# Performance work log

Measured on AMD Instinct MI355X. Metric: run time of the kernel, lower is better.

Reference implementation:

```python
import jax, jax.numpy as jnp
import numpy as np
import math

B = 2048
NOSC = 64            # oscillators per modality
M = 3                # modalities (audio, text, vision) in sorted order
BDIM = 256           # binding_dim
DT = 0.01
NSTEPS = 10
DIMS = [512, 768, 1024]  # audio, text, vision
TWO_PI = 2.0 * math.pi


def setup_inputs() -> dict:
    key = jax.random.key(0)
    ks = iter(jax.random.split(key, 40))
    d = {}
    names = ['a', 't', 'v']
    for name, dim, x_key in zip(names, DIMS, ['x_audio', 'x_text', 'x_vision']):
        d[x_key] = jax.random.normal(next(ks), (B, dim), dtype=jnp.float32)
        s = 1.0 / math.sqrt(dim)
        d[f'Wf_{name}'] = jax.random.uniform(next(ks), (BDIM, dim), jnp.float32, -s, s)
        d[f'bf_{name}'] = jax.random.uniform(next(ks), (BDIM,), jnp.float32, -s, s)
        d[f'Wp_{name}'] = jax.random.uniform(next(ks), (NOSC, dim), jnp.float32, -s, s)
        d[f'bp_{name}'] = jax.random.uniform(next(ks), (NOSC,), jnp.float32, -s, s)
    # omegas: randn*0.1 + 1.0 + i*0.5 for i-th sorted modality
    for i, name in enumerate(names):
        d[f'omega_{name}'] = jax.random.normal(next(ks), (NOSC,), jnp.float32) * 0.1 + 1.0 + i * 0.5
    N = M * NOSC
    d['inter_coupling'] = jax.random.normal(next(ks), (N, N), jnp.float32) * 0.1
    s = 1.0 / math.sqrt(BDIM * M)
    d['W_fusion'] = jax.random.uniform(next(ks), (BDIM, BDIM * M), jnp.float32, -s, s)
    d['b_fusion'] = jax.random.uniform(next(ks), (BDIM,), jnp.float32, -s, s)
    return d


def reference(x_audio, x_text, x_vision,
              Wf_a, bf_a, Wp_a, bp_a,
              Wf_t, bf_t, Wp_t, bp_t,
              Wf_v, bf_v, Wp_v, bp_v,
              omega_a, omega_t, omega_v,
              inter_coupling, W_fusion, b_fusion):
    def enc(x, Wf, bf, Wp, bp):
        encoded = x @ Wf.T + bf                       # (B, BDIM)
        phases = (x @ Wp.T + bp) % TWO_PI             # (B, NOSC)
        return encoded, phases

    e_a, p_a = enc(x_audio, Wf_a, bf_a, Wp_a, bp_a)
    e_t, p_t = enc(x_text, Wf_t, bf_t, Wp_t, bp_t)
    e_v, p_v = enc(x_vision, Wf_v, bf_v, Wp_v, bp_v)

    phases = jnp.concatenate([p_a, p_t, p_v], axis=-1)        # (B, N)
    omega = jnp.concatenate([omega_a, omega_t, omega_v])      # (N,)
    K = (inter_coupling + inter_coupling.T) * 0.5             # (N, N)
    N = phases.shape[-1]

    def step(ph, _):
        diff = ph[:, :, None] - ph[:, None, :]                # (B, N, N)
        forces = jnp.einsum('ij,bij->bi', K, jnp.sin(diff)) / N
        ph = (ph + DT * (omega[None, :] + forces)) % TWO_PI
        return ph, None

    phases, _ = jax.lax.scan(step, phases, None, length=NSTEPS)

    pm = [phases[:, i * NOSC:(i + 1) * NOSC] for i in range(M)]  # per-modality

    # PLV between banks a,b: |mean_{i,j} exp(i(a_i - b_j))| = R_a * R_b where
    # R = |mean_k exp(i phi_k)| (resultant length), computed with real math.
    R = jnp.stack([jnp.sqrt(jnp.mean(jnp.cos(p), -1) ** 2 +
                            jnp.mean(jnp.sin(p), -1) ** 2) for p in pm])  # (M, B)
    bm = jnp.mean(R[:, None, :] * R[None, :, :], axis=-1)      # (M, M)
    binding_matrix = jnp.where(jnp.eye(M, dtype=bool), 1.0, bm)

    fused_parts = []
    for e, p in zip([e_a, e_t, e_v], pm):
        phase_mod = jnp.mean(jnp.cos(p), axis=-1, keepdims=True)  # (B, 1)
        fused_parts.append(e * (0.5 + 0.5 * phase_mod))
    fused = jnp.concatenate(fused_parts, axis=-1)              # (B, M*BDIM)
    bound = fused @ W_fusion.T + b_fusion                      # (B, BDIM)

    triu = jnp.triu(jnp.ones((M, M), dtype=bool), k=1)
    total = jnp.sum(jnp.where(triu, binding_matrix, 0.0)) / triu.sum()
    total_binding = jnp.full((bound.shape[0],), total)

    return bound, binding_matrix, phases, total_binding
```

## Files before the change

kernel.cpp:

```cpp
#include <hip/hip_runtime.h>
#include <math.h>

typedef short bf16x8 __attribute__((ext_vector_type(8)));
typedef short bf16x4 __attribute__((ext_vector_type(4)));
typedef float f32x4  __attribute__((ext_vector_type(4)));

#define INV_2PI  0.15915494309189535f
#define TWO_PI_F 6.283185307179586f
#define FSCALE   8.2893199e-06f

static __device__ inline short f2bf(float f) {
    union { float f; unsigned u; } v; v.f = f;
    unsigned r = (v.u + 0x7FFFu + ((v.u >> 16) & 1u)) >> 16;
    return (short)r;
}
static __device__ inline float bf2f(short h) {
    union { unsigned u; float f; } v; v.u = ((unsigned)(unsigned short)h) << 16;
    return v.f;
}

__global__ __launch_bounds__(256) void front_kernel(
    const float* __restrict__ xa, const float* __restrict__ xt, const float* __restrict__ xv,
    const float* __restrict__ Wpa, const float* __restrict__ Wpt, const float* __restrict__ Wpv,
    const float* __restrict__ Wfa, const float* __restrict__ Wft, const float* __restrict__ Wfv,
    const float* __restrict__ Wfu,
    const float* __restrict__ IC,
    const float* __restrict__ oa, const float* __restrict__ ot, const float* __restrict__ ov,
    const float* __restrict__ bpa, const float* __restrict__ bpt, const float* __restrict__ bpv,
    float* __restrict__ partial, short* __restrict__ XB, short* __restrict__ WB,
    short* __restrict__ Kp,
    float* __restrict__ om_eff, float* __restrict__ bp_all, float* __restrict__ bacc)
{
    __shared__ alignas(16) float As[16][72];
    __shared__ alignas(16) float Bs[16][72];
    int b = blockIdx.x;
    int t = threadIdx.x;

    if (b < 576) {
        int slot = b % 18, rb = b / 18;
        int z = slot < 4 ? 0 : (slot < 10 ? 1 : 2);
        int chunk = slot - (z == 0 ? 0 : (z == 1 ? 4 : 10));
        const float* A = z == 0 ? xa : (z == 1 ? xt : xv);
        const float* W = z == 0 ? Wpa : (z == 1 ? Wpt : Wpv);
        short* XBz = XB + (z == 0 ? 0 : (z == 1 ? 1048576 : 2621440));
        int K = z == 0 ? 512 : (z == 1 ? 768 : 1024);
        int kb = chunk * 128;
        int m0 = rb * 64;

        int tx = t & 15, ty = t >> 4;
        int row = t >> 2, c4 = t & 3;

        float acc[4][4] = {};
        float4 ar = *(const float4*)&A[(size_t)(m0 + row) * K + kb + c4 * 4];
        float4 br = *(const float4*)&W[(size_t)row * K + kb + c4 * 4];

        for (int k0 = 0; k0 < 128; k0 += 16) {
            if (k0) __syncthreads();
            As[c4 * 4 + 0][row] = ar.x;
            As[c4 * 4 + 1][row] = ar.y;
            As[c4 * 4 + 2][row] = ar.z;
            As[c4 * 4 + 3][row] = ar.w;
            Bs[c4 * 4 + 0][row] = br.x;
            Bs[c4 * 4 + 1][row] = br.y;
            Bs[c4 * 4 + 2][row] = br.z;
            Bs[c4 * 4 + 3][row] = br.w;
            {
                bf16x4 h; h[0] = f2bf(ar.x); h[1] = f2bf(ar.y);
                h[2] = f2bf(ar.z); h[3] = f2bf(ar.w);
                *(bf16x4*)&XBz[(size_t)(m0 + row) * K + kb + k0 + c4 * 4] = h;
            }
            __syncthreads();
            if (k0 + 16 < 128) {
                ar = *(const float4*)&A[(size_t)(m0 + row) * K + kb + k0 + 16 + c4 * 4];
                br = *(const float4*)&W[(size_t)row * K + kb + k0 + 16 + c4 * 4];
            }
#pragma unroll
            for (int kk = 0; kk < 16; ++kk) {
                float4 aq = *(const float4*)&As[kk][ty * 4];
                float4 bq = *(const float4*)&Bs[kk][tx * 4];
                float av[4] = {aq.x, aq.y, aq.z, aq.w};
                float bv[4] = {bq.x, bq.y, bq.z, bq.w};
#pragma unroll
                for (int i = 0; i < 4; ++i)
#pragma unroll
                    for (int j = 0; j < 4; ++j)
                        acc[i][j] += av[i] * bv[j];
            }
        }

        float* P = partial + (size_t)slot * 131072;
#pragma unroll
        for (int i = 0; i < 4; ++i) {
            float4 v = make_float4(acc[i][0], acc[i][1], acc[i][2], acc[i][3]);
            *(float4*)&P[(size_t)(m0 + ty * 4 + i) * 64 + tx * 4] = v;
        }
    } else if (b < 600) {
        for (int u = (b - 576) * 256 + t; u < 196608; u += 24 * 256) {
            const float4* sp;
            if (u < 32768)       sp = (const float4*)Wfa + u;
            else if (u < 81920)  sp = (const float4*)Wft + (u - 32768);
            else if (u < 147456) sp = (const float4*)Wfv + (u - 81920);
            else                 sp = (const float4*)Wfu + (u - 147456);
            float4 v = *sp;
            bf16x4 h; h[0] = f2bf(v.x); h[1] = f2bf(v.y); h[2] = f2bf(v.z); h[3] = f2bf(v.w);
            *(bf16x4*)(WB + (size_t)u * 4) = h;
        }
    } else if (b < 632) {
        for (int idx = (b - 600) * 256 + t; idx < 36864; idx += 32 * 256) {
            int k = idx / 192, n = idx - k * 192;
            float v = 0.5f * (IC[k * 192 + n] + IC[n * 192 + k]);
            int nt = n >> 4, kc = k >> 5;
            int lane = ((k >> 3) & 3) * 16 + (n & 15);
            int j = k & 7;
            Kp[((nt * 6 + kc) * 64 + lane) * 8 + j] = f2bf(v);
        }
    } else {
        if (t < 192) {
            float w = t < 64 ? oa[t] : (t < 128 ? ot[t - 64] : ov[t - 128]);
            om_eff[t] = w * (0.01f * INV_2PI);
            float bb = t < 64 ? bpa[t] : (t < 128 ? bpt[t - 64] : bpv[t - 128]);
            bp_all[t] = bb;
        }
        if (t < 4) bacc[t] = 0.f;
    }
}

__global__ __launch_bounds__(256) void mid_kernel(
    const short* __restrict__ XB, const short* __restrict__ WB,
    const float* __restrict__ ba, const float* __restrict__ bt, const float* __restrict__ bv,
    const float* __restrict__ partial, const float* __restrict__ bp_all,
    const short* __restrict__ Kp, const float* __restrict__ om_eff,
    short* __restrict__ e_bf16,
    float* __restrict__ phases_out, float* __restrict__ pm, float* __restrict__ bacc)
{
    __shared__ alignas(16) char smem[27840];
    int b = blockIdx.x;
    int t = threadIdx.x;
    int lane = t & 63, w = t >> 6;
    int q = lane >> 4, col = lane & 15;

    if (b < 384) {
        int z = b / 128, r = b % 128;
        int m0 = (r >> 2) * 64, n0 = (r & 3) * 64;
        const short* A    = XB + (z == 0 ? 0 : (z == 1 ? 1048576 : 2621440));
        const short* W    = WB + (z == 0 ? 0 : (z == 1 ? 131072 : 327680));
        const float* bias = z == 0 ? ba : (z == 1 ? bt : bv);
        int K             = z == 0 ? 512 : (z == 1 ? 768 : 1024);

        short* As = (short*)smem;
        short* Bs = (short*)smem + 64 * 72;

        int srow = t >> 3, sc8 = t & 7;

        f32x4 acc[4];
#pragma unroll
        for (int f = 0; f < 4; ++f)
#pragma unroll
            for (int rr = 0; rr < 4; ++rr) acc[f][rr] = 0.f;

        bf16x8 av[2], bv8[2];
#pragma unroll
        for (int p = 0; p < 2; ++p) {
            av[p]  = *(const bf16x8*)&A[(size_t)(m0 + srow + 32 * p) * K + sc8 * 8];
            bv8[p] = *(const bf16x8*)&W[(size_t)(n0 + srow + 32 * p) * K + sc8 * 8];
        }

        for (int kb = 0; kb < K; kb += 64) {
            if (kb) __syncthreads();
#pragma unroll
            for (int p = 0; p < 2; ++p) {
                *(bf16x8*)&As[(srow + 32 * p) * 72 + sc8 * 8] = av[p];
                *(bf16x8*)&Bs[(srow + 32 * p) * 72 + sc8 * 8] = bv8[p];
            }
            __syncthreads();
            if (kb + 64 < K) {
#pragma unroll
                for (int p = 0; p < 2; ++p) {
                    av[p]  = *(const bf16x8*)&A[(size_t)(m0 + srow + 32 * p) * K + kb + 64 + sc8 * 8];
                    bv8[p] = *(const bf16x8*)&W[(size_t)(n0 + srow + 32 * p) * K + kb + 64 + sc8 * 8];
                }
            }

            bf16x8 bfr[2];
#pragma unroll
            for (int kc = 0; kc < 2; ++kc)
                bfr[kc] = *(const bf16x8*)&Bs[(w * 16 + col) * 72 + kc * 32 + q * 8];
#pragma unroll
            for (int f = 0; f < 4; ++f)
#pragma unroll
                for (int kc = 0; kc < 2; ++kc) {
                    bf16x8 af = *(const bf16x8*)&As[(f * 16 + col) * 72 + kc * 32 + q * 8];
                    acc[f] = __builtin_amdgcn_mfma_f32_16x16x32_bf16(af, bfr[kc], acc[f], 0, 0, 0);
                }
        }

        int n = n0 + w * 16 + col;
        float bn = bias[n];
#pragma unroll
        for (int f = 0; f < 4; ++f)
#pragma unroll
            for (int rr = 0; rr < 4; ++rr) {
                int m = m0 + f * 16 + q * 4 + rr;
                e_bf16[(size_t)m * 768 + z * 256 + n] = f2bf(acc[f][rr] + bn);
            }
    } else {
        short (*cs)[2][16][216] = (short (*)[2][16][216])smem;
        float (*Rl)[3] = (float (*)[3])(smem + 27648);

        int m0 = (b - 384) * 16;

        bf16x8 kb[3][6];
#pragma unroll
        for (int ntl = 0; ntl < 3; ++ntl)
#pragma unroll
            for (int kc = 0; kc < 6; ++kc) {
                int nt = w * 3 + ntl;
                kb[ntl][kc] = *(const bf16x8*)&Kp[((nt * 6 + kc) * 64 + lane) * 8];
            }

        float ph[3][4], om[3], c[3][4], s[3][4];
#pragma unroll
        for (int ntl = 0; ntl < 3; ++ntl) {
            int i = (w * 3 + ntl) * 16 + col;
            int z = i >> 6;
            int c0 = (z == 0) ? 0 : (z == 1 ? 4 : 10);
            int nch = (z == 0) ? 4 : (z == 1 ? 6 : 8);
            om[ntl] = om_eff[i];
#pragma unroll
            for (int r = 0; r < 4; ++r) {
                float raw = bp_all[i];
                size_t base = (size_t)c0 * 131072 + (size_t)(m0 + q * 4 + r) * 64 + (i & 63);
#pragma unroll
                for (int cc = 0; cc < 8; ++cc)
                    if (cc < nch) raw += partial[base + (size_t)cc * 131072];
                raw *= INV_2PI;
                ph[ntl][r] = raw - floorf(raw);
            }
        }

        for (int step = 0; step < 10; ++step) {
            int p = step & 1;
#pragma unroll
            for (int ntl = 0; ntl < 3; ++ntl) {
                int i = (w * 3 + ntl) * 16 + col;
#pragma unroll
                for (int r = 0; r < 4; ++r) {
                    c[ntl][r] = __builtin_amdgcn_cosf(ph[ntl][r]);
                    s[ntl][r] = __builtin_amdgcn_sinf(ph[ntl][r]);
                    cs[p][0][q * 4 + r][i] = f2bf(c[ntl][r]);
                    cs[p][1][q * 4 + r][i] = f2bf(s[ntl][r]);
                }
            }
            __syncthreads();

            f32x4 aC[3], aS[3];
#pragma unroll
            for (int ntl = 0; ntl < 3; ++ntl)
#pragma unroll
                for (int r = 0; r < 4; ++r) { aC[ntl][r] = 0.f; aS[ntl][r] = 0.f; }

#pragma unroll
            for (int kc = 0; kc < 6; ++kc) {
                bf16x8 ac  = *(const bf16x8*)&cs[p][0][col][kc * 32 + q * 8];
                bf16x8 as_ = *(const bf16x8*)&cs[p][1][col][kc * 32 + q * 8];
#pragma unroll
                for (int ntl = 0; ntl < 3; ++ntl) {
                    aC[ntl] = __builtin_amdgcn_mfma_f32_16x16x32_bf16(ac,  kb[ntl][kc], aC[ntl], 0, 0, 0);
                    aS[ntl] = __builtin_amdgcn_mfma_f32_16x16x32_bf16(as_, kb[ntl][kc], aS[ntl], 0, 0, 0);
                }
            }

#pragma unroll
            for (int ntl = 0; ntl < 3; ++ntl)
#pragma unroll
                for (int r = 0; r < 4; ++r) {
                    float f = (s[ntl][r] * aC[ntl][r] - c[ntl][r] * aS[ntl][r]) * FSCALE;
                    float pn = ph[ntl][r] + om[ntl] + f;
                    ph[ntl][r] = pn - floorf(pn);
                }
        }

#pragma unroll
        for (int ntl = 0; ntl < 3; ++ntl) {
            int i = (w * 3 + ntl) * 16 + col;
#pragma unroll
            for (int r = 0; r < 4; ++r) {
                float cp = __builtin_amdgcn_cosf(ph[ntl][r]);
                float sp = __builtin_amdgcn_sinf(ph[ntl][r]);
                cs[0][0][q * 4 + r][i] = f2bf(cp);
                cs[0][1][q * 4 + r][i] = f2bf(sp);
                phases_out[(size_t)(m0 + q * 4 + r) * 192 + i] = ph[ntl][r] * TWO_PI_F;
            }
        }
        __syncthreads();

        if (t < 48) {
            int r = t & 15, mod = t >> 4;
            float sc = 0.f, ss = 0.f;
#pragma unroll
            for (int g = 0; g < 8; ++g) {
                bf16x8 vc = *(const bf16x8*)&cs[0][0][r][mod * 64 + g * 8];
                bf16x8 vs = *(const bf16x8*)&cs[0][1][r][mod * 64 + g * 8];
#pragma unroll
                for (int j = 0; j < 8; ++j) { sc += bf2f(vc[j]); ss += bf2f(vs[j]); }
            }
            sc *= (1.f / 64.f); ss *= (1.f / 64.f);
            pm[(size_t)(m0 + r) * 3 + mod] = 0.5f + 0.5f * sc;
            Rl[r][mod] = sqrtf(sc * sc + ss * ss);
        }
        __syncthreads();
        if (t < 3) {
            int a = (t == 2) ? 1 : 0;
            int bb = (t == 0) ? 1 : 2;
            float accp = 0.f;
            for (int r = 0; r < 16; ++r) accp += Rl[r][a] * Rl[r][bb];
            atomicAdd(&bacc[t], accp);
        }
    }
}

__global__ __launch_bounds__(256) void back_kernel(
    const short* __restrict__ e_bf16, const short* __restrict__ WB,
    const float* __restrict__ bias, const float* __restrict__ pm,
    const float* __restrict__ bacc,
    float* __restrict__ out_bound, float* __restrict__ out_bm, float* __restrict__ out_total)
{
    const short* Wfb = WB + 589824;
    __shared__ alignas(16) short As2[16 * 776];

    int m0 = blockIdx.x * 16, n0 = blockIdx.y * 128;
    int t = threadIdx.x;
    int lane = t & 63, w = t >> 6;
    int q = lane >> 4, col = lane & 15;

#pragma unroll
    for (int i = 0; i < 6; ++i) {
        int g = t + 256 * i;
        int rw = g / 96, cg = g - rw * 96;
        float sc = pm[(size_t)(m0 + rw) * 3 + (cg >> 5)];
        bf16x8 v = *(const bf16x8*)&e_bf16[(size_t)(m0 + rw) * 768 + cg * 8];
        bf16x8 h;
#pragma unroll
        for (int j = 0; j < 8; ++j) h[j] = f2bf(bf2f(v[j]) * sc);
        *(bf16x8*)&As2[rw * 776 + cg * 8] = h;
    }
    __syncthreads();

    f32x4 facc[2];
#pragma unroll
    for (int j = 0; j < 2; ++j)
#pragma unroll
        for (int rr = 0; rr < 4; ++rr) facc[j][rr] = 0.f;

    int n_[2];
#pragma unroll
    for (int j = 0; j < 2; ++j) n_[j] = n0 + (w * 2 + j) * 16 + col;

    bf16x8 bcur[2], bnxt[2];
#pragma unroll
    for (int j = 0; j < 2; ++j)
        bcur[j] = *(const bf16x8*)&Wfb[(size_t)n_[j] * 768 + q * 8];

    for (int k0 = 0; k0 < 768; k0 += 32) {
        if (k0 + 32 < 768) {
#pragma unroll
            for (int j = 0; j < 2; ++j)
                bnxt[j] = *(const bf16x8*)&Wfb[(size_t)n_[j] * 768 + k0 + 32 + q * 8];
        }
        bf16x8 af = *(const bf16x8*)&As2[col * 776 + k0 + q * 8];
#pragma unroll
        for (int j = 0; j < 2; ++j)
            facc[j] = __builtin_amdgcn_mfma_f32_16x16x32_bf16(af, bcur[j], facc[j], 0, 0, 0);
#pragma unroll
        for (int j = 0; j < 2; ++j) bcur[j] = bnxt[j];
    }

#pragma unroll
    for (int j = 0; j < 2; ++j) {
        float bn = bias[n_[j]];
#pragma unroll
        for (int rr = 0; rr < 4; ++rr) {
            int m = m0 + q * 4 + rr;
            out_bound[(size_t)m * 256 + n_[j]] = facc[j][rr] + bn;
        }
    }

    if (blockIdx.x == 0 && blockIdx.y == 0) {
        float p01 = bacc[0] * (1.f / 2048.f);
        float p02 = bacc[1] * (1.f / 2048.f);
        float p12 = bacc[2] * (1.f / 2048.f);
        float total = (p01 + p02 + p12) * (1.f / 3.f);
        if (t == 0) {
            out_bm[0] = 1.f; out_bm[1] = p01; out_bm[2] = p02;
            out_bm[3] = p01; out_bm[4] = 1.f; out_bm[5] = p12;
            out_bm[6] = p02; out_bm[7] = p12; out_bm[8] = 1.f;
        }
        for (int i = t; i < 2048; i += 256) out_total[i] = total;
    }
}

extern "C" void kernel_launch(void* const* d_in, const int* in_sizes, int n_in,
                              void* d_out, int out_size, void* d_ws, size_t ws_size,
                              hipStream_t stream)
{
    const float* x_a  = (const float*)d_in[0];
    const float* Wf_a = (const float*)d_in[1];
    const float* bf_a = (const float*)d_in[2];
    const float* Wp_a = (const float*)d_in[3];
    const float* bp_a = (const float*)d_in[4];
    const float* x_t  = (const float*)d_in[5];
    const float* Wf_t = (const float*)d_in[6];
    const float* bf_t = (const float*)d_in[7];
    const float* Wp_t = (const float*)d_in[8];
    const float* bp_t = (const float*)d_in[9];
    const float* x_v  = (const float*)d_in[10];
    const float* Wf_v = (const float*)d_in[11];
    const float* bf_v = (const float*)d_in[12];
    const float* Wp_v = (const float*)d_in[13];
    const float* bp_v = (const float*)d_in[14];
    const float* om_a = (const float*)d_in[15];
    const float* om_t = (const float*)d_in[16];
    const float* om_v = (const float*)d_in[17];
    const float* IC   = (const float*)d_in[18];
    const float* Wfu  = (const float*)d_in[19];
    const float* bfu  = (const float*)d_in[20];

    float* ws      = (float*)d_ws;
    float* omw     = ws;
    float* bpw     = ws + 256;
    float* pmv     = ws + 512;
    float* baccw   = ws + 6656;
    float* partial = ws + 6720;
    short* e_bf    = (short*)(ws + 2366016);
    short* XB      = (short*)(ws + 3152448);
    short* Kpck    = (short*)(ws + 5511744);
    short* WB      = (short*)(ws + 5530176);

    float* out        = (float*)d_out;
    float* out_bound  = out;
    float* out_bm     = out + 524288;
    float* out_phases = out + 524297;
    float* out_total  = out + 917513;

    front_kernel<<<633, 256, 0, stream>>>(
        x_a, x_t, x_v, Wp_a, Wp_t, Wp_v, Wf_a, Wf_t, Wf_v, Wfu,
        IC, om_a, om_t, om_v, bp_a, bp_t, bp_v,
        partial, XB, WB, Kpck, omw, bpw, baccw);

    mid_kernel<<<512, 256, 0, stream>>>(
        XB, WB, bf_a, bf_t, bf_v,
        partial, bpw, Kpck, omw,
        e_bf, out_phases, pmv, baccw);

    dim3 gF(128, 2);
    back_kernel<<<gF, 256, 0, stream>>>(e_bf, WB, bfu, pmv, baccw,
                                        out_bound, out_bm, out_total);
}
```

Before: 158.8 us.

## Restructure phase GEMM tiles, split bf16 conversion into separate blocks, coalesce partial reduction

The phase-projection blocks now stage a full 64x64 k-slab into row-major shared memory with float4 loads, in two stages instead of eight. The bf16 conversion of the activations moves out of those GEMM blocks into dedicated conversion blocks, which also convert the weights. The split-K partials are stored in a blocked layout, so the oscillator blocks can reduce them with coalesced vector loads through shared memory, and those blocks are reordered to run first in mid_kernel. The changes aim to cut uncoalesced partial reads and per-iteration syncs, at the cost of more front-kernel blocks and more shared memory per block.

```diff
diff --git a/kernel.cpp b/kernel.cpp
--- a/kernel.cpp
+++ b/kernel.cpp
@@ -31,8 +31,8 @@
     short* __restrict__ Kp,
     float* __restrict__ om_eff, float* __restrict__ bp_all, float* __restrict__ bacc)
 {
-    __shared__ alignas(16) float As[16][72];
-    __shared__ alignas(16) float Bs[16][72];
+    __shared__ alignas(16) float As[64][68];
+    __shared__ alignas(16) float Bs[64][68];
     int b = blockIdx.x;
     int t = threadIdx.x;
 
@@ -42,71 +42,87 @@
         int chunk = slot - (z == 0 ? 0 : (z == 1 ? 4 : 10));
         const float* A = z == 0 ? xa : (z == 1 ? xt : xv);
         const float* W = z == 0 ? Wpa : (z == 1 ? Wpt : Wpv);
-        short* XBz = XB + (z == 0 ? 0 : (z == 1 ? 1048576 : 2621440));
         int K = z == 0 ? 512 : (z == 1 ? 768 : 1024);
         int kb = chunk * 128;
         int m0 = rb * 64;
 
         int tx = t & 15, ty = t >> 4;
-        int row = t >> 2, c4 = t & 3;
+        int srow = t >> 4, sk4 = t & 15;
 
         float acc[4][4] = {};
-        float4 ar = *(const float4*)&A[(size_t)(m0 + row) * K + kb + c4 * 4];
-        float4 br = *(const float4*)&W[(size_t)row * K + kb + c4 * 4];
-
-        for (int k0 = 0; k0 < 128; k0 += 16) {
-            if (k0) __syncthreads();
-            As[c4 * 4 + 0][row] = ar.x;
-            As[c4 * 4 + 1][row] = ar.y;
-            As[c4 * 4 + 2][row] = ar.z;
-            As[c4 * 4 + 3][row] = ar.w;
-            Bs[c4 * 4 + 0][row] = br.x;
-            Bs[c4 * 4 + 1][row] = br.y;
-            Bs[c4 * 4 + 2][row] = br.z;
-            Bs[c4 * 4 + 3][row] = br.w;
-            {
-                bf16x4 h; h[0] = f2bf(ar.x); h[1] = f2bf(ar.y);
-                h[2] = f2bf(ar.z); h[3] = f2bf(ar.w);
-                *(bf16x4*)&XBz[(size_t)(m0 + row) * K + kb + k0 + c4 * 4] = h;
+
+        float4 ar[4], br[4];
+#pragma unroll
+        for (int p = 0; p < 4; ++p) {
+            ar[p] = *(const float4*)&A[(size_t)(m0 + srow + 16 * p) * K + kb + sk4 * 4];
+            br[p] = *(const float4*)&W[(size_t)(srow + 16 * p) * K + kb + sk4 * 4];
+        }
+
+        for (int st = 0; st < 2; ++st) {
+            if (st) __syncthreads();
+#pragma unroll
+            for (int p = 0; p < 4; ++p) {
+                *(float4*)&As[srow + 16 * p][sk4 * 4] = ar[p];
+                *(float4*)&Bs[srow + 16 * p][sk4 * 4] = br[p];
             }
             __syncthreads();
-            if (k0 + 16 < 128) {
-                ar = *(const float4*)&A[(size_t)(m0 + row) * K + kb + k0 + 16 + c4 * 4];
-                br = *(const float4*)&W[(size_t)row * K + kb + k0 + 16 + c4 * 4];
-            }
-#pragma unroll
-            for (int kk = 0; kk < 16; ++kk) {
-                float4 aq = *(const float4*)&As[kk][ty * 4];
-                float4 bq = *(const float4*)&Bs[kk][tx * 4];
-                float av[4] = {aq.x, aq.y, aq.z, aq.w};
-                float bv[4] = {bq.x, bq.y, bq.z, bq.w};
+            if (st == 0) {
+#pragma unroll
+                for (int p = 0; p < 4; ++p) {
+                    ar[p] = *(const float4*)&A[(size_t)(m0 + srow + 16 * p) * K + kb + 64 + sk4 * 4];
+                    br[p] = *(const float4*)&W[(size_t)(srow + 16 * p) * K + kb + 64 + sk4 * 4];
+                }
+            }
+#pragma unroll
+            for (int k4 = 0; k4 < 16; ++k4) {
+                float4 a4[4], b4[4];
+#pragma unroll
+                for (int i = 0; i < 4; ++i) a4[i] = *(const float4*)&As[ty * 4 + i][k4 * 4];
+#pragma unroll
+                for (int j = 0; j < 4; ++j) b4[j] = *(const float4*)&Bs[tx * 4 + j][k4 * 4];
 #pragma unroll
                 for (int i = 0; i < 4; ++i)
 #pragma unroll
-                    for (int j = 0; j < 4; ++j)
-                        acc[i][j] += av[i] * bv[j];
-            }
-        }
-
-        float* P = partial + (size_t)slot * 131072;
+                    for (int j = 0; j < 4; ++j) {
+                        acc[i][j] += a4[i].x * b4[j].x;
+                        acc[i][j] += a4[i].y * b4[j].y;
+                        acc[i][j] += a4[i].z * b4[j].z;
+                        acc[i][j] += a4[i].w * b4[j].w;
+                    }
+            }
+        }
+
 #pragma unroll
         for (int i = 0; i < 4; ++i) {
+            int row = ty * 4 + i;
+            int qb = rb * 4 + (row >> 4), rloc = row & 15;
             float4 v = make_float4(acc[i][0], acc[i][1], acc[i][2], acc[i][3]);
-            *(float4*)&P[(size_t)(m0 + ty * 4 + i) * 64 + tx * 4] = v;
-        }
-    } else if (b < 600) {
-        for (int u = (b - 576) * 256 + t; u < 196608; u += 24 * 256) {
-            const float4* sp;
-            if (u < 32768)       sp = (const float4*)Wfa + u;
-            else if (u < 81920)  sp = (const float4*)Wft + (u - 32768);
-            else if (u < 147456) sp = (const float4*)Wfv + (u - 81920);
-            else                 sp = (const float4*)Wfu + (u - 147456);
-            float4 v = *sp;
-            bf16x4 h; h[0] = f2bf(v.x); h[1] = f2bf(v.y); h[2] = f2bf(v.z); h[3] = f2bf(v.w);
-            *(bf16x4*)(WB + (size_t)u * 4) = h;
-        }
-    } else if (b < 632) {
-        for (int idx = (b - 600) * 256 + t; idx < 36864; idx += 32 * 256) {
+            *(float4*)&partial[((size_t)(qb * 18 + slot)) * 1024 + rloc * 64 + tx * 4] = v;
+        }
+    } else if (b < 672) {
+        for (int u = (b - 576) * 256 + t; u < 1376256; u += 96 * 256) {
+            if (u < 1179648) {
+                const float4* sp;
+                if (u < 262144)      sp = (const float4*)xa + u;
+                else if (u < 655360) sp = (const float4*)xt + (u - 262144);
+                else                 sp = (const float4*)xv + (u - 655360);
+                float4 v = *sp;
+                bf16x4 h; h[0] = f2bf(v.x); h[1] = f2bf(v.y); h[2] = f2bf(v.z); h[3] = f2bf(v.w);
+                *(bf16x4*)&XB[(size_t)u * 4] = h;
+            } else {
+                int uw = u - 1179648;
+                const float4* sp;
+                if (uw < 32768)       sp = (const float4*)Wfa + uw;
+                else if (uw < 81920)  sp = (const float4*)Wft + (uw - 32768);
+                else if (uw < 147456) sp = (const float4*)Wfv + (uw - 81920);
+                else                  sp = (const float4*)Wfu + (uw - 147456);
+                float4 v = *sp;
+                bf16x4 h; h[0] = f2bf(v.x); h[1] = f2bf(v.y); h[2] = f2bf(v.z); h[3] = f2bf(v.w);
+                *(bf16x4*)(WB + (size_t)uw * 4) = h;
+            }
+        }
+    } else if (b < 704) {
+        for (int idx = (b - 672) * 256 + t; idx < 36864; idx += 32 * 256) {
             int k = idx / 192, n = idx - k * 192;
             float v = 0.5f * (IC[k * 192 + n] + IC[n * 192 + k]);
             int nt = n >> 4, kc = k >> 5;
@@ -139,8 +155,9 @@
     int lane = t & 63, w = t >> 6;
     int q = lane >> 4, col = lane & 15;
 
-    if (b < 384) {
-        int z = b / 128, r = b % 128;
+    if (b >= 128) {
+        int bb = b - 128;
+        int z = bb / 128, r = bb % 128;
         int m0 = (r >> 2) * 64, n0 = (r & 3) * 64;
         const short* A    = XB + (z == 0 ? 0 : (z == 1 ? 1048576 : 2621440));
         const short* W    = WB + (z == 0 ? 0 : (z == 1 ? 131072 : 327680));
@@ -206,8 +223,9 @@
     } else {
         short (*cs)[2][16][216] = (short (*)[2][16][216])smem;
         float (*Rl)[3] = (float (*)[3])(smem + 27648);
-
-        int m0 = (b - 384) * 16;
+        float* ph0 = (float*)smem;
+
+        int m0 = b * 16;
 
         bf16x8 kb[3][6];
 #pragma unroll
@@ -218,25 +236,38 @@
                 kb[ntl][kc] = *(const bf16x8*)&Kp[((nt * 6 + kc) * 64 + lane) * 8];
             }
 
+        {
+            const float* Pb = partial + (size_t)b * 18 * 1024;
+            f32x4 s0, s1, s2;
+#pragma unroll
+            for (int j = 0; j < 4; ++j) { s0[j] = 0.f; s1[j] = 0.f; s2[j] = 0.f; }
+#pragma unroll
+            for (int s = 0; s < 18; ++s) {
+                f32x4 v = *(const f32x4*)&Pb[s * 1024 + t * 4];
+                if (s < 4)       s0 += v;
+                else if (s < 10) s1 += v;
+                else             s2 += v;
+            }
+            int row = t >> 4, c4 = t & 15;
+            *(f32x4*)&ph0[row * 196 +   0 + c4 * 4] = s0;
+            *(f32x4*)&ph0[row * 196 +  64 + c4 * 4] = s1;
+            *(f32x4*)&ph0[row * 196 + 128 + c4 * 4] = s2;
+        }
+        __syncthreads();
+
         float ph[3][4], om[3], c[3][4], s[3][4];
 #pragma unroll
         for (int ntl = 0; ntl < 3; ++ntl) {
             int i = (w * 3 + ntl) * 16 + col;
-            int z = i >> 6;
-            int c0 = (z == 0) ? 0 : (z == 1 ? 4 : 10);
-            int nch = (z == 0) ? 4 : (z == 1 ? 6 : 8);
             om[ntl] = om_eff[i];
 #pragma unroll
             for (int r = 0; r < 4; ++r) {
-                float raw = bp_all[i];
-                size_t base = (size_t)c0 * 131072 + (size_t)(m0 + q * 4 + r) * 64 + (i & 63);
-#pragma unroll
-                for (int cc = 0; cc < 8; ++cc)
-                    if (cc < nch) raw += partial[base + (size_t)cc * 131072];
+                float raw = bp_all[i] + ph0[(q * 4 + r) * 196 + i];
                 raw *= INV_2PI;
                 ph[ntl][r] = raw - floorf(raw);
             }
         }
+        __syncthreads();
 
         for (int step = 0; step < 10; ++step) {
             int p = step & 1;
@@ -442,7 +473,7 @@
     float* out_phases = out + 524297;
     float* out_total  = out + 917513;
 
-    front_kernel<<<633, 256, 0, stream>>>(
+    front_kernel<<<705, 256, 0, stream>>>(
         x_a, x_t, x_v, Wp_a, Wp_t, Wp_v, Wf_a, Wf_t, Wf_v, Wfu,
         IC, om_a, om_t, om_v, bp_a, bp_t, bp_v,
         partial, XB, WB, Kpck, omw, bpw, baccw);
```

New measurement: 172.6 us. +8.7%, slower.

## Tile split-K phase partials per row block and reorder mid-kernel block roles

Applied to the files above, without the earlier changes.

The front kernel now writes split-K phase partials in a layout grouped by 16-row block, with all 18 K-slices for a row block stored contiguously. The oscillator blocks in the mid kernel then read them with coalesced float4 loads, reduce per modality, and stage the sums in shared memory, replacing strided scalar gathers across 131072-float slabs. The oscillator blocks also move to the low block indices so they are scheduled first, ahead of the encoder GEMM blocks. This adds an extra shared-memory staging pass and two barriers.

```diff
diff --git a/kernel.cpp b/kernel.cpp
--- a/kernel.cpp
+++ b/kernel.cpp
@@ -88,11 +88,12 @@
             }
         }
 
-        float* P = partial + (size_t)slot * 131072;
 #pragma unroll
         for (int i = 0; i < 4; ++i) {
+            int row_l = ty * 4 + i;
+            int qb = rb * 4 + (row_l >> 4), rloc = row_l & 15;
             float4 v = make_float4(acc[i][0], acc[i][1], acc[i][2], acc[i][3]);
-            *(float4*)&P[(size_t)(m0 + ty * 4 + i) * 64 + tx * 4] = v;
+            *(float4*)&partial[((size_t)(qb * 18 + slot)) * 1024 + rloc * 64 + tx * 4] = v;
         }
     } else if (b < 600) {
         for (int u = (b - 576) * 256 + t; u < 196608; u += 24 * 256) {
@@ -139,8 +140,9 @@
     int lane = t & 63, w = t >> 6;
     int q = lane >> 4, col = lane & 15;
 
-    if (b < 384) {
-        int z = b / 128, r = b % 128;
+    if (b >= 128) {
+        int bb = b - 128;
+        int z = bb / 128, r = bb % 128;
         int m0 = (r >> 2) * 64, n0 = (r & 3) * 64;
         const short* A    = XB + (z == 0 ? 0 : (z == 1 ? 1048576 : 2621440));
         const short* W    = WB + (z == 0 ? 0 : (z == 1 ? 131072 : 327680));
@@ -206,8 +208,9 @@
     } else {
         short (*cs)[2][16][216] = (short (*)[2][16][216])smem;
         float (*Rl)[3] = (float (*)[3])(smem + 27648);
-
-        int m0 = (b - 384) * 16;
+        float* ph0 = (float*)smem;
+
+        int m0 = b * 16;
 
         bf16x8 kb[3][6];
 #pragma unroll
@@ -218,25 +221,38 @@
                 kb[ntl][kc] = *(const bf16x8*)&Kp[((nt * 6 + kc) * 64 + lane) * 8];
             }
 
+        {
+            const float* Pb = partial + (size_t)b * 18 * 1024;
+            f32x4 s0, s1, s2;
+#pragma unroll
+            for (int j = 0; j < 4; ++j) { s0[j] = 0.f; s1[j] = 0.f; s2[j] = 0.f; }
+#pragma unroll
+            for (int s = 0; s < 18; ++s) {
+                f32x4 v = *(const f32x4*)&Pb[s * 1024 + t * 4];
+                if (s < 4)       s0 += v;
+                else if (s < 10) s1 += v;
+                else             s2 += v;
+            }
+            int row = t >> 4, c4 = t & 15;
+            *(f32x4*)&ph0[row * 196 +   0 + c4 * 4] = s0;
+            *(f32x4*)&ph0[row * 196 +  64 + c4 * 4] = s1;
+            *(f32x4*)&ph0[row * 196 + 128 + c4 * 4] = s2;
+        }
+        __syncthreads();
+
         float ph[3][4], om[3], c[3][4], s[3][4];
 #pragma unroll
         for (int ntl = 0; ntl < 3; ++ntl) {
             int i = (w * 3 + ntl) * 16 + col;
-            int z = i >> 6;
-            int c0 = (z == 0) ? 0 : (z == 1 ? 4 : 10);
-            int nch = (z == 0) ? 4 : (z == 1 ? 6 : 8);
             om[ntl] = om_eff[i];
 #pragma unroll
             for (int r = 0; r < 4; ++r) {
-                float raw = bp_all[i];
-                size_t base = (size_t)c0 * 131072 + (size_t)(m0 + q * 4 + r) * 64 + (i & 63);
-#pragma unroll
-                for (int cc = 0; cc < 8; ++cc)
-                    if (cc < nch) raw += partial[base + (size_t)cc * 131072];
+                float raw = bp_all[i] + ph0[(q * 4 + r) * 196 + i];
                 raw *= INV_2PI;
                 ph[ntl][r] = raw - floorf(raw);
             }
         }
+        __syncthreads();
 
         for (int step = 0; step < 10; ++step) {
             int p = step & 1;
```

Result: faster. 142.3 us (-10.4%).
